# Kernel tuning notes

Hardware: AMD Instinct MI355X
Metric: run time of the kernel (lower is better)

## Reference

```python
import jax, jax.numpy as jnp
import numpy as np

N = 100000      # nodes
R = 8           # relations
E_DIM = 128     # embedding dim
N_EDGES = 1600000  # n * avg_degree(16)


def setup_inputs() -> dict:
    key = jax.random.key(0)
    k1, k2, k3, k4, k5 = jax.random.split(key, 5)
    x = jax.random.normal(k1, (N, E_DIM), dtype=jnp.float32)
    # xavier-ish scale for (r, e, e) relation weights
    weights = jax.random.normal(k2, (R, E_DIM, E_DIM), dtype=jnp.float32) * (1.0 / np.sqrt(E_DIM))
    edge_rel = jax.random.randint(k3, (N_EDGES,), 0, R, dtype=jnp.int32)
    edge_src = jax.random.randint(k4, (N_EDGES,), 0, N, dtype=jnp.int32)
    edge_dst = jax.random.randint(k5, (N_EDGES,), 0, N, dtype=jnp.int32)
    return dict(x=x, weights=weights, edge_rel=edge_rel, edge_src=edge_src, edge_dst=edge_dst)


def reference(x, weights, edge_rel, edge_src, edge_dst):
    n, e = x.shape
    r = weights.shape[0]
    # sparse adjacency row index: relation-block row = rel * n + dst  (shape rn)
    rows = edge_rel.astype(jnp.int32) * n + edge_dst.astype(jnp.int32)
    # row-normalized values: vals = 1 / row_degree (util.sum_sparse)
    deg = jax.ops.segment_sum(jnp.ones(rows.shape, dtype=x.dtype), rows, num_segments=r * n)
    vals = 1.0 / deg[rows]  # only evaluated at rows with >=1 edge
    # SpMM: h = graph @ x, viewed as (r, n, e)
    msgs = vals[:, None] * x[edge_src]                       # (E, e) gather
    h = jax.ops.segment_sum(msgs, rows, num_segments=r * n)  # (r*n, e) scatter-add
    h = h.reshape(r, n, e)
    # per-relation transform: (r, e_out, e_in) x (r, n, e_in) -> (n, r, e_out)
    h = jnp.einsum('rih,rnh->nri', weights, h)
    # SumUnify: relu(sum over relations)
    return jax.nn.relu(h.sum(axis=1))
```

## Files before the change

kernel.cpp:

```cpp
#include <hip/hip_runtime.h>
#include <hip/hip_bf16.h>

#define ED 128
#define RR 8
#define KTOT (RR * ED)
#define LDB 136
#define CH 50048

typedef __attribute__((ext_vector_type(8))) short short8;
typedef __attribute__((ext_vector_type(4))) float f32x4;
typedef __attribute__((ext_vector_type(4))) unsigned short u16x4;

#define RL(v, i) __builtin_amdgcn_readlane(v, i)

__device__ __forceinline__ unsigned short f2bf(float f){
  unsigned int u = __builtin_bit_cast(unsigned int, f);
  return (unsigned short)((u + 0x7fffu + ((u >> 16) & 1u)) >> 16);
}
__device__ __forceinline__ float bf2f(unsigned int lo){
  return __builtin_bit_cast(float, lo << 16);
}
__device__ __forceinline__ unsigned int packbf(float hi, float lo){
  return ((unsigned int)f2bf(hi) << 16) | f2bf(lo);
}

__global__ void cast_bf16_vec(const float* __restrict__ in, unsigned short* __restrict__ out, int n4){
  int stride = gridDim.x * blockDim.x;
  for (int i = blockIdx.x * blockDim.x + threadIdx.x; i < n4; i += stride){
    f32x4 v = __builtin_nontemporal_load((const f32x4*)(in + (size_t)i * 4));
    u16x4 o;
    o[0] = f2bf(v[0]); o[1] = f2bf(v[1]); o[2] = f2bf(v[2]); o[3] = f2bf(v[3]);
    *(u16x4*)(out + (size_t)i * 4) = o;
  }
}

__global__ void hist_rank(const int* __restrict__ rel, const int* __restrict__ dst,
                          int* __restrict__ rowcnt, int* __restrict__ rank, int E){
  int stride = gridDim.x * blockDim.x;
  for (int i = blockIdx.x * blockDim.x + threadIdx.x; i < E; i += stride)
    rank[i] = atomicAdd(&rowcnt[(dst[i] << 3) | rel[i]], 1);
}

__launch_bounds__(1024)
__global__ void scan_block_sum(const int* __restrict__ rowcnt, int* __restrict__ bsum, int m){
  __shared__ int lds[16];
  int t = threadIdx.x;
  int idx = blockIdx.x * 1024 + t;
  int v = (idx < m) ? rowcnt[idx] : 0;
#pragma unroll
  for (int o = 32; o > 0; o >>= 1) v += __shfl_down(v, o);
  if ((t & 63) == 0) lds[t >> 6] = v;
  __syncthreads();
  if (t == 0){
    int s = 0;
#pragma unroll
    for (int w = 0; w < 16; ++w) s += lds[w];
    bsum[blockIdx.x] = s;
  }
}

__launch_bounds__(1024)
__global__ void scan_bsum_par(const int* __restrict__ bsum, int* __restrict__ bscan,
                              int nb, int* __restrict__ total_out){
  __shared__ int wsum[16];
  int t = threadIdx.x, lane = t & 63, wid = t >> 6;
  int v = (t < nb) ? bsum[t] : 0;
  int incl = v;
#pragma unroll
  for (int o = 1; o < 64; o <<= 1){
    int u = __shfl_up(incl, o);
    if (lane >= o) incl += u;
  }
  if (lane == 63) wsum[wid] = incl;
  __syncthreads();
  int woff = 0;
  for (int w0 = 0; w0 < wid; ++w0) woff += wsum[w0];
  if (t < nb) bscan[t] = woff + incl - v;
  if (t == nb - 1) *total_out = woff + incl;
}

__launch_bounds__(1024)
__global__ void scan_final(const int* __restrict__ rowcnt, const int* __restrict__ bscan,
                           int* __restrict__ row_ptr, int m){
  __shared__ int wsum[16];
  int t = threadIdx.x, lane = t & 63, wid = t >> 6;
  int idx = blockIdx.x * 1024 + t;
  int v = (idx < m) ? rowcnt[idx] : 0;
  int incl = v;
#pragma unroll
  for (int o = 1; o < 64; o <<= 1){
    int u = __shfl_up(incl, o);
    if (lane >= o) incl += u;
  }
  if (lane == 63) wsum[wid] = incl;
  __syncthreads();
  int woff = bscan[blockIdx.x];
  for (int w0 = 0; w0 < wid; ++w0) woff += wsum[w0];
  if (idx < m) row_ptr[idx] = woff + incl - v;
}

__global__ void scatter_pos(const int* __restrict__ rel, const int* __restrict__ src,
                            const int* __restrict__ dst, const int* __restrict__ rank,
                            const int* __restrict__ row_ptr, int* __restrict__ payload, int E){
  int stride = gridDim.x * blockDim.x;
  for (int i = blockIdx.x * blockDim.x + threadIdx.x; i < E; i += stride){
    int key = (dst[i] << 3) | rel[i];
    payload[row_ptr[key] + rank[i]] = src[i];
  }
}

__launch_bounds__(256)
__global__ void row_agg(const unsigned short* __restrict__ xb,
                        const int* __restrict__ row_ptr8,
                        const int* __restrict__ payload,
                        unsigned short* __restrict__ h2buf, int d0, int d1){
  int d    = d0 + ((blockIdx.x * 256 + threadIdx.x) >> 6);
  int lane = threadIdx.x & 63;
  if (d >= d1) return;

  int p9 = 0;
  if (lane < 9) p9 = row_ptr8[(d << 3) + lane];
  int b0  = RL(p9, 0);
  int o1  = RL(p9, 1) - b0;
  int o2  = RL(p9, 2) - b0;
  int o3  = RL(p9, 3) - b0;
  int o4  = RL(p9, 4) - b0;
  int o5  = RL(p9, 5) - b0;
  int o6  = RL(p9, 6) - b0;
  int o7  = RL(p9, 7) - b0;
  int cnt = RL(p9, 8) - b0;

  float ax0=0.f,ay0=0.f,ax1=0.f,ay1=0.f,ax2=0.f,ay2=0.f,ax3=0.f,ay3=0.f;
  float ax4=0.f,ay4=0.f,ax5=0.f,ay5=0.f,ax6=0.f,ay6=0.f,ax7=0.f,ay7=0.f;

#define ROUTE(VV, IDX) { \
    float lo = bf2f((VV) & 0xffffu), hi = bf2f((VV) >> 16); \
    if ((IDX) < o4){ \
      if ((IDX) < o2){ if ((IDX) < o1){ ax0+=lo; ay0+=hi; } else { ax1+=lo; ay1+=hi; } } \
      else           { if ((IDX) < o3){ ax2+=lo; ay2+=hi; } else { ax3+=lo; ay3+=hi; } } \
    } else { \
      if ((IDX) < o6){ if ((IDX) < o5){ ax4+=lo; ay4+=hi; } else { ax5+=lo; ay5+=hi; } } \
      else           { if ((IDX) < o7){ ax6+=lo; ay6+=hi; } else { ax7+=lo; ay7+=hi; } } \
    } }

  if (cnt <= 64){
    int pl = payload[b0 + lane];
    int e = 0;
    for (; e + 8 <= cnt; e += 8){
      int s0 = RL(pl, e);
      int s1 = RL(pl, e + 1);
      int s2 = RL(pl, e + 2);
      int s3 = RL(pl, e + 3);
      int s4 = RL(pl, e + 4);
      int s5 = RL(pl, e + 5);
      int s6 = RL(pl, e + 6);
      int s7 = RL(pl, e + 7);
      unsigned int v0 = ((const unsigned int*)(xb + ((size_t)s0 << 7)))[lane];
      unsigned int v1 = ((const unsigned int*)(xb + ((size_t)s1 << 7)))[lane];
      unsigned int v2 = ((const unsigned int*)(xb + ((size_t)s2 << 7)))[lane];
      unsigned int v3 = ((const unsigned int*)(xb + ((size_t)s3 << 7)))[lane];
      unsigned int v4 = ((const unsigned int*)(xb + ((size_t)s4 << 7)))[lane];
      unsigned int v5 = ((const unsigned int*)(xb + ((size_t)s5 << 7)))[lane];
      unsigned int v6 = ((const unsigned int*)(xb + ((size_t)s6 << 7)))[lane];
      unsigned int v7 = ((const unsigned int*)(xb + ((size_t)s7 << 7)))[lane];
      ROUTE(v0, e)
      ROUTE(v1, e + 1)
      ROUTE(v2, e + 2)
      ROUTE(v3, e + 3)
      ROUTE(v4, e + 4)
      ROUTE(v5, e + 5)
      ROUTE(v6, e + 6)
      ROUTE(v7, e + 7)
    }
    for (; e < cnt; ++e){
      int s = RL(pl, e);
      unsigned int v = ((const unsigned int*)(xb + ((size_t)s << 7)))[lane];
      ROUTE(v, e)
    }
  } else {
    for (int e = 0; e < cnt; ++e){
      int s = __builtin_amdgcn_readfirstlane(payload[b0 + e]);
      unsigned int v = ((const unsigned int*)(xb + ((size_t)s << 7)))[lane];
      ROUTE(v, e)
    }
  }
#undef ROUTE

  int c0 = o1, c1 = o2 - o1, c2 = o3 - o2, c3 = o4 - o3;
  int c4 = o5 - o4, c5 = o6 - o5, c6 = o7 - o6, c7 = cnt - o7;
  unsigned int* hp = (unsigned int*)h2buf + ((size_t)(d - d0) << 9) + lane;
  float sc;
  sc = c0 ? 1.f / (float)c0 : 0.f; hp[0]   = packbf(ay0*sc, ax0*sc);
  sc = c1 ? 1.f / (float)c1 : 0.f; hp[64]  = packbf(ay1*sc, ax1*sc);
  sc = c2 ? 1.f / (float)c2 : 0.f; hp[128] = packbf(ay2*sc, ax2*sc);
  sc = c3 ? 1.f / (float)c3 : 0.f; hp[192] = packbf(ay3*sc, ax3*sc);
  sc = c4 ? 1.f / (float)c4 : 0.f; hp[256] = packbf(ay4*sc, ax4*sc);
  sc = c5 ? 1.f / (float)c5 : 0.f; hp[320] = packbf(ay5*sc, ax5*sc);
  sc = c6 ? 1.f / (float)c6 : 0.f; hp[384] = packbf(ay6*sc, ax6*sc);
  sc = c7 ? 1.f / (float)c7 : 0.f; hp[448] = packbf(ay7*sc, ax7*sc);
}

__launch_bounds__(256)
__global__ void gemm_out(const unsigned short* __restrict__ h2buf,
                         const unsigned short* __restrict__ wbb,
                         float* __restrict__ out, int d0, int d1){
  __shared__ __align__(16) unsigned short lds_a[128 * LDB];
  __shared__ __align__(16) unsigned short lds_b[128 * LDB];
  const int t = threadIdx.x;
  const int wave = t >> 6, lane = t & 63;
  const int wr = wave >> 1, wc = wave & 1;
  const int dbase = d0 + blockIdx.x * 128;
  const int frow = lane & 15, kb = lane >> 4;

  f32x4 acc[4][4];
#pragma unroll
  for (int rt = 0; rt < 4; ++rt)
#pragma unroll
    for (int jt = 0; jt < 4; ++jt)
      acc[rt][jt] = (f32x4){0.f, 0.f, 0.f, 0.f};

  short8 pa[8], pb[8];
#pragma unroll
  for (int p = 0; p < 8; ++p){
    int q = p * 256 + t;
    int row = q >> 4, col = q & 15;
    int gr = dbase + row; if (gr >= d1) gr = d1 - 1;
    pa[p] = *(const short8*)(h2buf + (size_t)(gr - d0) * KTOT + col * 8);
    pb[p] = *(const short8*)(wbb + row * ED + col * 8);
  }

  for (int r = 0; r < RR; ++r){
    __syncthreads();
#pragma unroll
    for (int p = 0; p < 8; ++p){
      int q = p * 256 + t;
      int row = q >> 4, col = q & 15;
      *(short8*)&lds_a[row * LDB + col * 8] = pa[p];
      *(short8*)&lds_b[row * LDB + col * 8] = pb[p];
    }
    __syncthreads();

    if (r + 1 < RR){
#pragma unroll
      for (int p = 0; p < 8; ++p){
        int q = p * 256 + t;
        int row = q >> 4, col = q & 15;
        int gr = dbase + row; if (gr >= d1) gr = d1 - 1;
        pa[p] = *(const short8*)(h2buf + (size_t)(gr - d0) * KTOT + (r + 1) * ED + col * 8);
        pb[p] = *(const short8*)(wbb + (size_t)(r + 1) * ED * ED + row * ED + col * 8);
      }
    }

    short8 a[4][4], b[4][4];
#pragma unroll
    for (int rt = 0; rt < 4; ++rt)
#pragma unroll
      for (int ks = 0; ks < 4; ++ks)
        a[rt][ks] = *(const short8*)&lds_a[(wr * 64 + rt * 16 + frow) * LDB + ks * 32 + kb * 8];
#pragma unroll
    for (int jt = 0; jt < 4; ++jt)
#pragma unroll
      for (int ks = 0; ks < 4; ++ks)
        b[jt][ks] = *(const short8*)&lds_b[(wc * 64 + jt * 16 + frow) * LDB + ks * 32 + kb * 8];
#pragma unroll
    for (int rt = 0; rt < 4; ++rt)
#pragma unroll
      for (int jt = 0; jt < 4; ++jt)
#pragma unroll
        for (int ks = 0; ks < 4; ++ks)
          acc[rt][jt] = __builtin_amdgcn_mfma_f32_16x16x32_bf16(a[rt][ks], b[jt][ks], acc[rt][jt], 0, 0, 0);
  }

  const int drow = (lane >> 4) * 4;
  const int dcol = lane & 15;
#pragma unroll
  for (int rt = 0; rt < 4; ++rt)
#pragma unroll
    for (int jt = 0; jt < 4; ++jt)
#pragma unroll
      for (int reg = 0; reg < 4; ++reg){
        int i = dbase + wr * 64 + rt * 16 + drow + reg;
        if (i < d1)
          __builtin_nontemporal_store(fmaxf(acc[rt][jt][reg], 0.f),
                                      &out[(size_t)i * ED + wc * 64 + jt * 16 + dcol]);
      }
}

extern "C" void kernel_launch(void* const* d_in, const int* in_sizes, int n_in,
                              void* d_out, int out_size, void* d_ws, size_t ws_size,
                              hipStream_t stream){
  const float* x  = (const float*)d_in[0];
  const float* w  = (const float*)d_in[1];
  const int* erel = (const int*)d_in[2];
  const int* esrc = (const int*)d_in[3];
  const int* edst = (const int*)d_in[4];
  float* out = (float*)d_out;

  const int n = in_sizes[0] / ED;
  const int E = in_sizes[2];
  const int m = n * RR;
  const int NB = (m + 1023) / 1024;

  char* ws = (char*)d_ws;
  size_t off = 0;
  auto alloc = [&](size_t bytes) -> char* {
    char* p = ws + off;
    off += (bytes + 255) & ~(size_t)255;
    return p;
  };
  unsigned short* h2buf   = (unsigned short*)alloc((size_t)CH * KTOT * 2);
  unsigned short* xb      = (unsigned short*)alloc((size_t)n * ED * 2);
  unsigned short* wbb     = (unsigned short*)alloc((size_t)RR * ED * ED * 2);
  int*            payload = (int*)alloc((size_t)E * 4);
  int*            row_ptr = (int*)alloc((size_t)(m + 1) * 4);
  int*            rowcnt  = (int*)alloc((size_t)m * 4);
  int*            rank    = (int*)alloc((size_t)E * 4);
  int*            bsum    = (int*)alloc((size_t)NB * 4);
  int*            bscan   = (int*)alloc((size_t)NB * 4);
  if (off > ws_size || NB > 1024) return;

  (void)hipMemsetAsync(rowcnt, 0, (size_t)m * 4, stream);

  cast_bf16_vec<<<2048, 256, 0, stream>>>(x, xb, n * ED / 4);
  cast_bf16_vec<<<128, 256, 0, stream>>>(w, wbb, RR * ED * ED / 4);
  hist_rank    <<<2048, 256, 0, stream>>>(erel, edst, rowcnt, rank, E);
  scan_block_sum<<<NB, 1024, 0, stream>>>(rowcnt, bsum, m);
  scan_bsum_par<<<1, 1024, 0, stream>>>(bsum, bscan, NB, row_ptr + m);
  scan_final   <<<NB, 1024, 0, stream>>>(rowcnt, bscan, row_ptr, m);
  scatter_pos  <<<2048, 256, 0, stream>>>(erel, esrc, edst, rank, row_ptr, payload, E);

  for (int c = 0; c < 2; ++c){
    int d0 = c * CH;
    int d1 = (c == 0) ? CH : n;
    int nodes = d1 - d0;
    row_agg <<<(nodes + 3) / 4, 256, 0, stream>>>(xb, row_ptr, payload, h2buf, d0, d1);
    gemm_out<<<(nodes + 127) / 128, 256, 0, stream>>>(h2buf, wbb, out, d0, d1);
  }
}
```

Baseline: 285.8 us.

## Fuse casts with histogram, pack row counters as 16-bit pairs, vectorize edge loops

```diff
diff --git a/kernel.cpp b/kernel.cpp
--- a/kernel.cpp
+++ b/kernel.cpp
@@ -6,6 +6,9 @@
 #define KTOT (RR * ED)
 #define LDB 136
 #define CH 50048
+#define HB 1568
+#define CB 1600
+#define WB 8
 
 typedef __attribute__((ext_vector_type(8))) short short8;
 typedef __attribute__((ext_vector_type(4))) float f32x4;
@@ -23,30 +26,60 @@
 __device__ __forceinline__ unsigned int packbf(float hi, float lo){
   return ((unsigned int)f2bf(hi) << 16) | f2bf(lo);
 }
-
-__global__ void cast_bf16_vec(const float* __restrict__ in, unsigned short* __restrict__ out, int n4){
-  int stride = gridDim.x * blockDim.x;
-  for (int i = blockIdx.x * blockDim.x + threadIdx.x; i < n4; i += stride){
-    f32x4 v = __builtin_nontemporal_load((const f32x4*)(in + (size_t)i * 4));
-    u16x4 o;
-    o[0] = f2bf(v[0]); o[1] = f2bf(v[1]); o[2] = f2bf(v[2]); o[3] = f2bf(v[3]);
-    *(u16x4*)(out + (size_t)i * 4) = o;
-  }
-}
-
-__global__ void hist_rank(const int* __restrict__ rel, const int* __restrict__ dst,
-                          int* __restrict__ rowcnt, int* __restrict__ rank, int E){
-  int stride = gridDim.x * blockDim.x;
-  for (int i = blockIdx.x * blockDim.x + threadIdx.x; i < E; i += stride)
-    rank[i] = atomicAdd(&rowcnt[(dst[i] << 3) | rel[i]], 1);
+__device__ __forceinline__ void cast4(const float* __restrict__ in,
+                                      unsigned short* __restrict__ out, int i){
+  f32x4 v = __builtin_nontemporal_load((const f32x4*)(in + (size_t)i * 4));
+  u16x4 o;
+  o[0] = f2bf(v[0]); o[1] = f2bf(v[1]); o[2] = f2bf(v[2]); o[3] = f2bf(v[3]);
+  *(u16x4*)(out + (size_t)i * 4) = o;
+}
+
+__global__ void fused_front(const int* __restrict__ rel, const int* __restrict__ dst,
+                            unsigned int* __restrict__ rowcnt, int* __restrict__ rank,
+                            const float* __restrict__ x, unsigned short* __restrict__ xb, int nx4,
+                            const float* __restrict__ w, unsigned short* __restrict__ wb, int nw4,
+                            int E){
+  int b = blockIdx.x;
+  if (b < HB){
+    int tid = b * 256 + threadIdx.x;
+    int nthr = HB * 256;
+    int E4 = E >> 2;
+    for (int i = tid; i < E4; i += nthr){
+      int4 r4 = ((const int4*)rel)[i];
+      int4 d4 = ((const int4*)dst)[i];
+      int k0 = (d4.x << 3) | r4.x;
+      int k1 = (d4.y << 3) | r4.y;
+      int k2 = (d4.z << 3) | r4.z;
+      int k3 = (d4.w << 3) | r4.w;
+      unsigned o0 = atomicAdd(&rowcnt[k0 >> 1], (k0 & 1) ? 0x10000u : 1u);
+      unsigned o1 = atomicAdd(&rowcnt[k1 >> 1], (k1 & 1) ? 0x10000u : 1u);
+      unsigned o2 = atomicAdd(&rowcnt[k2 >> 1], (k2 & 1) ? 0x10000u : 1u);
+      unsigned o3 = atomicAdd(&rowcnt[k3 >> 1], (k3 & 1) ? 0x10000u : 1u);
+      int4 rk;
+      rk.x = (k0 & 1) ? (int)(o0 >> 16) : (int)(o0 & 0xffffu);
+      rk.y = (k1 & 1) ? (int)(o1 >> 16) : (int)(o1 & 0xffffu);
+      rk.z = (k2 & 1) ? (int)(o2 >> 16) : (int)(o2 & 0xffffu);
+      rk.w = (k3 & 1) ? (int)(o3 >> 16) : (int)(o3 & 0xffffu);
+      ((int4*)rank)[i] = rk;
+    }
+  } else if (b < HB + CB){
+    int tid = (b - HB) * 256 + threadIdx.x;
+    int nthr = CB * 256;
+    for (int i = tid; i < nx4; i += nthr) cast4(x, xb, i);
+  } else {
+    int tid = (b - HB - CB) * 256 + threadIdx.x;
+    int nthr = WB * 256;
+    for (int i = tid; i < nw4; i += nthr) cast4(w, wb, i);
+  }
 }
 
 __launch_bounds__(1024)
-__global__ void scan_block_sum(const int* __restrict__ rowcnt, int* __restrict__ bsum, int m){
+__global__ void scan_block_sum(const unsigned int* __restrict__ rowcnt, int* __restrict__ bsum, int mm){
   __shared__ int lds[16];
   int t = threadIdx.x;
   int idx = blockIdx.x * 1024 + t;
-  int v = (idx < m) ? rowcnt[idx] : 0;
+  unsigned pv = (idx < mm) ? rowcnt[idx] : 0u;
+  int v = (int)(pv & 0xffffu) + (int)(pv >> 16);
 #pragma unroll
   for (int o = 32; o > 0; o >>= 1) v += __shfl_down(v, o);
   if ((t & 63) == 0) lds[t >> 6] = v;
@@ -80,12 +113,14 @@
 }
 
 __launch_bounds__(1024)
-__global__ void scan_final(const int* __restrict__ rowcnt, const int* __restrict__ bscan,
-                           int* __restrict__ row_ptr, int m){
+__global__ void scan_final(const unsigned int* __restrict__ rowcnt, const int* __restrict__ bscan,
+                           int* __restrict__ row_ptr, int mm){
   __shared__ int wsum[16];
   int t = threadIdx.x, lane = t & 63, wid = t >> 6;
   int idx = blockIdx.x * 1024 + t;
-  int v = (idx < m) ? rowcnt[idx] : 0;
+  unsigned pv = (idx < mm) ? rowcnt[idx] : 0u;
+  int lo = (int)(pv & 0xffffu);
+  int v = lo + (int)(pv >> 16);
   int incl = v;
 #pragma unroll
   for (int o = 1; o < 64; o <<= 1){
@@ -96,16 +131,32 @@
   __syncthreads();
   int woff = bscan[blockIdx.x];
   for (int w0 = 0; w0 < wid; ++w0) woff += wsum[w0];
-  if (idx < m) row_ptr[idx] = woff + incl - v;
+  if (idx < mm){
+    int ex = woff + incl - v;
+    row_ptr[2 * idx]     = ex;
+    row_ptr[2 * idx + 1] = ex + lo;
+  }
 }
 
 __global__ void scatter_pos(const int* __restrict__ rel, const int* __restrict__ src,
                             const int* __restrict__ dst, const int* __restrict__ rank,
                             const int* __restrict__ row_ptr, int* __restrict__ payload, int E){
-  int stride = gridDim.x * blockDim.x;
-  for (int i = blockIdx.x * blockDim.x + threadIdx.x; i < E; i += stride){
-    int key = (dst[i] << 3) | rel[i];
-    payload[row_ptr[key] + rank[i]] = src[i];
+  int tid = blockIdx.x * 256 + threadIdx.x;
+  int nthr = gridDim.x * 256;
+  int E4 = E >> 2;
+  for (int i = tid; i < E4; i += nthr){
+    int4 r4 = ((const int4*)rel)[i];
+    int4 s4 = ((const int4*)src)[i];
+    int4 d4 = ((const int4*)dst)[i];
+    int4 k4 = ((const int4*)rank)[i];
+    int p0 = row_ptr[(d4.x << 3) | r4.x] + k4.x;
+    int p1 = row_ptr[(d4.y << 3) | r4.y] + k4.y;
+    int p2 = row_ptr[(d4.z << 3) | r4.z] + k4.z;
+    int p3 = row_ptr[(d4.w << 3) | r4.w] + k4.w;
+    payload[p0] = s4.x;
+    payload[p1] = s4.y;
+    payload[p2] = s4.z;
+    payload[p3] = s4.w;
   }
 }
 
@@ -299,7 +350,8 @@
   const int n = in_sizes[0] / ED;
   const int E = in_sizes[2];
   const int m = n * RR;
-  const int NB = (m + 1023) / 1024;
+  const int mm = m / 2;
+  const int NB = (mm + 1023) / 1024;
 
   char* ws = (char*)d_ws;
   size_t off = 0;
@@ -313,21 +365,21 @@
   unsigned short* wbb     = (unsigned short*)alloc((size_t)RR * ED * ED * 2);
   int*            payload = (int*)alloc((size_t)E * 4);
   int*            row_ptr = (int*)alloc((size_t)(m + 1) * 4);
-  int*            rowcnt  = (int*)alloc((size_t)m * 4);
+  unsigned int*   rowcnt  = (unsigned int*)alloc((size_t)mm * 4);
   int*            rank    = (int*)alloc((size_t)E * 4);
   int*            bsum    = (int*)alloc((size_t)NB * 4);
   int*            bscan   = (int*)alloc((size_t)NB * 4);
   if (off > ws_size || NB > 1024) return;
 
-  (void)hipMemsetAsync(rowcnt, 0, (size_t)m * 4, stream);
-
-  cast_bf16_vec<<<2048, 256, 0, stream>>>(x, xb, n * ED / 4);
-  cast_bf16_vec<<<128, 256, 0, stream>>>(w, wbb, RR * ED * ED / 4);
-  hist_rank    <<<2048, 256, 0, stream>>>(erel, edst, rowcnt, rank, E);
-  scan_block_sum<<<NB, 1024, 0, stream>>>(rowcnt, bsum, m);
+  (void)hipMemsetAsync(rowcnt, 0, (size_t)mm * 4, stream);
+
+  fused_front  <<<HB + CB + WB, 256, 0, stream>>>(erel, edst, rowcnt, rank,
+                                                  x, xb, n * ED / 4,
+                                                  w, wbb, RR * ED * ED / 4, E);
+  scan_block_sum<<<NB, 1024, 0, stream>>>(rowcnt, bsum, mm);
   scan_bsum_par<<<1, 1024, 0, stream>>>(bsum, bscan, NB, row_ptr + m);
-  scan_final   <<<NB, 1024, 0, stream>>>(rowcnt, bscan, row_ptr, m);
-  scatter_pos  <<<2048, 256, 0, stream>>>(erel, esrc, edst, rank, row_ptr, payload, E);
+  scan_final   <<<NB, 1024, 0, stream>>>(rowcnt, bscan, row_ptr, mm);
+  scatter_pos  <<<1568, 256, 0, stream>>>(erel, esrc, edst, rank, row_ptr, payload, E);
 
   for (int c = 0; c < 2; ++c){
     int d0 = c * CH;
```

New measurement: 283.8 us. No clear change (-0.7%).
